# Performance work log

Hardware: AMD Instinct MI355X
Metric: run time of the kernel (lower is better)

The kernel has to match this reference:

```python
import jax, jax.numpy as jnp
import numpy as np

B, NUM_SLOTS, D, TOP_K = 2048, 128, 1024, 8
DH = D // 2  # route_mlp hidden


def setup_inputs() -> dict:
    key = jax.random.key(0)
    ks = jax.random.split(key, 16)
    s = 0.02
    return {
        "x": jax.random.normal(ks[0], (B, D), jnp.float32),
        "S": jax.random.normal(ks[1], (B, NUM_SLOTS, D), jnp.float32),
        # route_mlp: Linear(2D, D//2) -> GELU -> Linear(D//2, NUM_SLOTS)
        "w1": jax.random.normal(ks[2], (DH, 2 * D), jnp.float32) * s,
        "b1": jnp.zeros((DH,), jnp.float32),
        "w2": jax.random.normal(ks[3], (NUM_SLOTS, DH), jnp.float32) * s,
        "b2": jnp.zeros((NUM_SLOTS,), jnp.float32),
        # GRUCell(D, D): torch layout, gates ordered (r, z, n)
        "gru_wih": jax.random.normal(ks[4], (3 * D, D), jnp.float32) * s,
        "gru_whh": jax.random.normal(ks[5], (3 * D, D), jnp.float32) * s,
        "gru_bih": jnp.zeros((3 * D,), jnp.float32),
        "gru_bhh": jnp.zeros((3 * D,), jnp.float32),
        "wval": jax.random.normal(ks[6], (D, D), jnp.float32) * s,
        "bval": jnp.zeros((D,), jnp.float32),
        "wout": jax.random.normal(ks[7], (D, D), jnp.float32) * s,
        "bout": jnp.zeros((D,), jnp.float32),
        "tau": jnp.ones((1,), jnp.float32),
    }


def reference(x, S, w1, b1, w2, b2, gru_wih, gru_whh, gru_bih, gru_bhh,
              wval, bval, wout, bout, tau):
    # Routing: context = [x, mean over slots]
    slot_mean = S.mean(axis=1)                                  # [B, D]
    ctx = jnp.concatenate([x, slot_mean], axis=-1)              # [B, 2D]
    h = jax.nn.gelu(ctx @ w1.T + b1, approximate=False)         # [B, DH]
    route_logits = (h @ w2.T + b2) / (jnp.abs(tau) + 0.1)       # [B, NUM_SLOTS]

    topk_vals, topk_idx = jax.lax.top_k(route_logits, TOP_K)    # [B, K]
    topk_w = jax.nn.softmax(topk_vals, axis=-1)                 # [B, K]

    # Gather selected slot states
    slot_states = jnp.take_along_axis(S, topk_idx[:, :, None], axis=1)  # [B, K, D]

    # GRUCell (torch semantics). Input part shared across the K slots.
    gi = x @ gru_wih.T + gru_bih                                # [B, 3D]
    gh = slot_states @ gru_whh.T + gru_bhh                      # [B, K, 3D]
    gi_r, gi_z, gi_n = jnp.split(gi, 3, axis=-1)
    gh_r, gh_z, gh_n = jnp.split(gh, 3, axis=-1)
    r = jax.nn.sigmoid(gi_r[:, None, :] + gh_r)
    z = jax.nn.sigmoid(gi_z[:, None, :] + gh_z)
    n = jnp.tanh(gi_n[:, None, :] + r * gh_n)
    updated = (1.0 - z) * n + z * slot_states                   # [B, K, D]

    # Scatter updated states back into slot memory
    S_new = S.at[jnp.arange(B)[:, None], topk_idx].set(updated)

    # Weighted value readout
    values = updated @ wval.T + bval                            # [B, K, D]
    mixed = jnp.einsum('bkd,bk->bd', values, topk_w)            # [B, D]
    output = mixed @ wout.T + bout                              # [B, D]
    return output, S_new
```

## Files before the change

### kernel.cpp

```cpp
#include <hip/hip_runtime.h>
#include <math.h>
#include <stdint.h>

#define B_   2048
#define NS_  128
#define D_   1024
#define K_   8
#define DH_  512
#define G3_  3072

typedef unsigned short u16;
typedef short bf16x8 __attribute__((ext_vector_type(8)));
typedef float f32x4 __attribute__((ext_vector_type(4)));

__device__ __forceinline__ float bf2f(u16 u) {
  union { unsigned i; float f; } v; v.i = ((unsigned)u) << 16; return v.f;
}
__device__ __forceinline__ u16 f2bf(float f) {
  unsigned x = __float_as_uint(f);
  return (u16)((x + 0x7fffu + ((x >> 16) & 1u)) >> 16);
}

#define AS1C(p) ((const __attribute__((address_space(1))) void*)(uintptr_t)(p))
#define AS3(p)  ((__attribute__((address_space(3))) void*)(unsigned)(uintptr_t)(p))

template<int DO_COPY>
__global__ __launch_bounds__(256)
void sp_copyprep(const float* __restrict__ S, float* __restrict__ Snew,
                 float* __restrict__ mean,
                 const float* __restrict__ x, const float* __restrict__ wih,
                 const float* __restrict__ whh, const float* __restrict__ wout,
                 const float* __restrict__ wval, const float* __restrict__ bval,
                 const float* __restrict__ bout,
                 u16* __restrict__ xb, u16* __restrict__ wihb,
                 u16* __restrict__ whhb, u16* __restrict__ woutb,
                 u16* __restrict__ wvalT, float* __restrict__ brow) {
  __shared__ u16 tile[64][65];
  const int blk = blockIdx.x;
  const int t = threadIdx.x;
  if (blk < 2048) {
    const int b = blk;
    const int d0 = t * 4;
    const f32x4* src = (const f32x4*)(S + (size_t)b * NS_ * D_) + t;
    f32x4* dst = (f32x4*)(Snew + (size_t)b * NS_ * D_) + t;
    double a0 = 0, a1 = 0, a2 = 0, a3 = 0;
    #pragma unroll 4
    for (int s = 0; s < NS_; ++s) {
      f32x4 v = __builtin_nontemporal_load(src);
      if (DO_COPY) __builtin_nontemporal_store(v, dst);
      a0 += v[0]; a1 += v[1]; a2 += v[2]; a3 += v[3];
      src += 256; dst += 256;
    }
    float4 m;
    m.x = (float)(a0 * (1.0 / 128.0)); m.y = (float)(a1 * (1.0 / 128.0));
    m.z = (float)(a2 * (1.0 / 128.0)); m.w = (float)(a3 * (1.0 / 128.0));
    *(float4*)&mean[(size_t)b * D_ + d0] = m;
  } else if (blk < 3072) {
    const int cid = blk - 2048;
    for (int i = cid * 256 + t; i < 2359296; i += 1024 * 256) {
      const float* s; u16* d; int off;
      if (i < 524288)       { s = x;    d = xb;    off = i; }
      else if (i < 1310720) { s = wih;  d = wihb;  off = i - 524288; }
      else if (i < 2097152) { s = whh;  d = whhb;  off = i - 1310720; }
      else                  { s = wout; d = woutb; off = i - 2097152; }
      float4 v = ((const float4*)s)[off];
      ushort4 o;
      o.x = f2bf(v.x); o.y = f2bf(v.y); o.z = f2bf(v.z); o.w = f2bf(v.w);
      ((ushort4*)d)[off] = o;
    }
  } else if (blk < 3328) {
    const int tb = blk - 3072;
    const int bx = tb & 15, by = tb >> 4;
    const int r = t >> 4, c4 = (t & 15) * 4;
    #pragma unroll
    for (int p = 0; p < 4; ++p) {
      const int row = by * 64 + p * 16 + r;
      float4 v = *(const float4*)&wval[(size_t)row * D_ + bx * 64 + c4];
      tile[p * 16 + r][c4 + 0] = f2bf(v.x);
      tile[p * 16 + r][c4 + 1] = f2bf(v.y);
      tile[p * 16 + r][c4 + 2] = f2bf(v.z);
      tile[p * 16 + r][c4 + 3] = f2bf(v.w);
    }
    __syncthreads();
    #pragma unroll
    for (int p = 0; p < 4; ++p) {
      const int jr = p * 16 + r;
      ushort4 o;
      o.x = tile[c4 + 0][jr];
      o.y = tile[c4 + 1][jr];
      o.z = tile[c4 + 2][jr];
      o.w = tile[c4 + 3][jr];
      *(ushort4*)&wvalT[(size_t)(bx * 64 + jr) * D_ + by * 64 + c4] = o;
    }
  } else {
    const int w = t >> 6, l = t & 63;
    const int i = (blk - 3328) * 4 + w;
    float s = 0.f;
    const float* wr = &wout[(size_t)i * D_ + l * 16];
    const float* bv = &bval[l * 16];
    #pragma unroll
    for (int j = 0; j < 16; j += 4) {
      float4 w4 = *(const float4*)&wr[j];
      float4 b4 = *(const float4*)&bv[j];
      s += w4.x * b4.x + w4.y * b4.y + w4.z * b4.z + w4.w * b4.w;
    }
    #pragma unroll
    for (int off = 32; off > 0; off >>= 1) s += __shfl_xor(s, off);
    if (l == 0) brow[i] = s + bout[i];
  }
}

template<int EPI>
__device__ __forceinline__ void gemm_bf16_body(
    const u16* __restrict__ A, const u16* __restrict__ Bm,
    void* __restrict__ Cv, const float* __restrict__ bias,
    int M, int N, int Kd, int nbx, int wg, u16* lA, u16* lB) {
  {
    const int nwg = nbx * ((M + 127) >> 7);
    const int cpx = nwg >> 3;
    wg = (wg & 7) * cpx + (wg >> 3);
  }
  const int m0 = (wg / nbx) * 128, n0 = (wg % nbx) * 128;
  const int t = threadIdx.x;
  const int lane = t & 63;
  const int w = t >> 6;
  const int wm = w >> 1, wn = w & 1;

  f32x4 acc[4][4] = {};

  const int srow = t >> 2;
  const int scol = (t & 3) * 8;
  const u16* gA0 = A + (size_t)(m0 + srow) * Kd + scol;
  const u16* gA1 = A + (size_t)(m0 + 64 + srow) * Kd + scol;
  const u16* gB0 = Bm + (size_t)(n0 + srow) * Kd + scol;
  const u16* gB1 = Bm + (size_t)(n0 + 64 + srow) * Kd + scol;
  u16* lAw = lA + (t & 192) * 8;
  u16* lBw = lB + (t & 192) * 8;

  const int kb = (lane >> 4) * 8;
  const int rA = wm * 64 + (lane & 15);
  const int rB = wn * 64 + (lane & 15);

  for (int k0 = 0; k0 < Kd; k0 += 32) {
    __builtin_amdgcn_global_load_lds(AS1C(gA0 + k0), AS3(lAw), 16, 0, 0);
    __builtin_amdgcn_global_load_lds(AS1C(gA1 + k0), AS3(lAw + 2048), 16, 0, 0);
    __builtin_amdgcn_global_load_lds(AS1C(gB0 + k0), AS3(lBw), 16, 0, 0);
    __builtin_amdgcn_global_load_lds(AS1C(gB1 + k0), AS3(lBw + 2048), 16, 0, 0);
    __syncthreads();
    bf16x8 af[4], bfr[4];
    #pragma unroll
    for (int fm = 0; fm < 4; ++fm)
      af[fm] = *(const bf16x8*)&lA[(rA + fm * 16) * 32 + kb];
    #pragma unroll
    for (int fn = 0; fn < 4; ++fn)
      bfr[fn] = *(const bf16x8*)&lB[(rB + fn * 16) * 32 + kb];
    #pragma unroll
    for (int fm = 0; fm < 4; ++fm) {
      #pragma unroll
      for (int fn = 0; fn < 4; ++fn)
        acc[fm][fn] = __builtin_amdgcn_mfma_f32_16x16x32_bf16(af[fm], bfr[fn], acc[fm][fn], 0, 0, 0);
    }
    __syncthreads();
  }

  #pragma unroll
  for (int fm = 0; fm < 4; ++fm) {
    #pragma unroll
    for (int fn = 0; fn < 4; ++fn) {
      #pragma unroll
      for (int i = 0; i < 4; ++i) {
        const int r = m0 + wm * 64 + fm * 16 + (lane >> 4) * 4 + i;
        const int c = n0 + wn * 64 + fn * 16 + (lane & 15);
        float v = acc[fm][fn][i];
        if constexpr (EPI == 2) {
          ((float*)Cv)[(size_t)r * N + c] = v + bias[c];
        } else {
          ((u16*)Cv)[(size_t)r * N + c] = f2bf(v);
        }
      }
    }
  }
}

__global__ __launch_bounds__(256)
void sp_mid(const u16* __restrict__ xb, const u16* __restrict__ wihb,
            u16* __restrict__ gib,
            const float* __restrict__ x, const float* __restrict__ mean,
            const float* __restrict__ w1, const float* __restrict__ b1,
            float* __restrict__ h,
            const u16* __restrict__ woutb, const u16* __restrict__ wvalTb,
            u16* __restrict__ Wrob) {
  __shared__ u16 lA[128 * 32];
  __shared__ u16 lB[128 * 32];
  const int blk = blockIdx.x;
  const int t = threadIdx.x;
  if (blk < 384) {
    gemm_bf16_body<1>(xb, wihb, gib, nullptr, B_, G3_, D_, G3_ / 128, blk, lA, lB);
  } else if (blk < 640) {
    float (*As)[68] = (float(*)[68])lA;
    float (*Bs)[68] = (float(*)[68])lB;
    int wg = blk - 384;
    wg = (wg & 7) * 32 + (wg >> 3);
    const int m0 = (wg >> 3) * 64;
    const int n0 = (wg & 7) * 64;
    const int tx = t & 15, ty = t >> 4;
    float acc[4][4] = {};
    const int sr = t >> 2, sc = (t & 3) * 4;
    for (int k0 = 0; k0 < 2 * D_; k0 += 16) {
      const float* src = (k0 < D_) ? (x + k0) : (mean + (k0 - D_));
      float4 va = *(const float4*)&src[(size_t)(m0 + sr) * D_ + sc];
      As[sc + 0][sr] = va.x; As[sc + 1][sr] = va.y; As[sc + 2][sr] = va.z; As[sc + 3][sr] = va.w;
      float4 vb = *(const float4*)&w1[(size_t)(n0 + sr) * (2 * D_) + k0 + sc];
      Bs[sc + 0][sr] = vb.x; Bs[sc + 1][sr] = vb.y; Bs[sc + 2][sr] = vb.z; Bs[sc + 3][sr] = vb.w;
      __syncthreads();
      #pragma unroll
      for (int kk = 0; kk < 16; ++kk) {
        float4 a4 = *(const float4*)&As[kk][ty * 4];
        float4 b4 = *(const float4*)&Bs[kk][tx * 4];
        acc[0][0] = fmaf(a4.x, b4.x, acc[0][0]); acc[0][1] = fmaf(a4.x, b4.y, acc[0][1]);
        acc[0][2] = fmaf(a4.x, b4.z, acc[0][2]); acc[0][3] = fmaf(a4.x, b4.w, acc[0][3]);
        acc[1][0] = fmaf(a4.y, b4.x, acc[1][0]); acc[1][1] = fmaf(a4.y, b4.y, acc[1][1]);
        acc[1][2] = fmaf(a4.y, b4.z, acc[1][2]); acc[1][3] = fmaf(a4.y, b4.w, acc[1][3]);
        acc[2][0] = fmaf(a4.z, b4.x, acc[2][0]); acc[2][1] = fmaf(a4.z, b4.y, acc[2][1]);
        acc[2][2] = fmaf(a4.z, b4.z, acc[2][2]); acc[2][3] = fmaf(a4.z, b4.w, acc[2][3]);
        acc[3][0] = fmaf(a4.w, b4.x, acc[3][0]); acc[3][1] = fmaf(a4.w, b4.y, acc[3][1]);
        acc[3][2] = fmaf(a4.w, b4.z, acc[3][2]); acc[3][3] = fmaf(a4.w, b4.w, acc[3][3]);
      }
      __syncthreads();
    }
    #pragma unroll
    for (int i = 0; i < 4; ++i) {
      #pragma unroll
      for (int j = 0; j < 4; ++j) {
        const int r = m0 + ty * 4 + i, c = n0 + tx * 4 + j;
        float v = acc[i][j] + b1[c];
        v = 0.5f * v * (1.0f + erff(v * 0.70710678118654752f));
        h[(size_t)r * DH_ + c] = v;
      }
    }
  } else {
    gemm_bf16_body<1>(woutb, wvalTb, Wrob, nullptr, D_, D_, D_, 8, blk - 640, lA, lB);
  }
}

__global__ __launch_bounds__(64)
void sp_route_topk(const float* __restrict__ h, const float* __restrict__ w2,
                   const float* __restrict__ b2, const float* __restrict__ tau,
                   const float* __restrict__ S,
                   int* __restrict__ tki, float* __restrict__ tkw,
                   u16* __restrict__ slotb) {
  __shared__ float hs[DH_];
  __shared__ int sTki[K_];
  const int b = blockIdx.x, l = threadIdx.x;
  *(float4*)&hs[l * 4] = *(const float4*)&h[(size_t)b * DH_ + l * 4];
  *(float4*)&hs[256 + l * 4] = *(const float4*)&h[(size_t)b * DH_ + 256 + l * 4];
  __syncthreads();
  const double invd = 1.0 / ((double)fabsf(tau[0]) + 0.1);
  float v[2]; int id[2];
  #pragma unroll
  for (int c = 0; c < 2; ++c) {
    const int n = c * 64 + l;
    const float* wr = &w2[(size_t)n * DH_];
    double s = 0.0;
    for (int j = 0; j < DH_; j += 4) {
      float4 w4 = *(const float4*)&wr[j];
      s += (double)hs[j] * (double)w4.x;
      s += (double)hs[j + 1] * (double)w4.y;
      s += (double)hs[j + 2] * (double)w4.z;
      s += (double)hs[j + 3] * (double)w4.w;
    }
    v[c] = (float)((s + (double)b2[n]) * invd);
    id[c] = n;
  }
  float m0f = 0.f, sum = 0.f, mye = 0.f; int myi = 0;
  for (int r = 0; r < 8; ++r) {
    float mv; int mi;
    if (v[1] > v[0]) { mv = v[1]; mi = id[1]; } else { mv = v[0]; mi = id[0]; }
    #pragma unroll
    for (int off = 32; off > 0; off >>= 1) {
      float ov = __shfl_xor(mv, off);
      int oi = __shfl_xor(mi, off);
      if (ov > mv || (ov == mv && oi < mi)) { mv = ov; mi = oi; }
    }
    if (r == 0) m0f = mv;
    float er = expf(mv - m0f);
    sum += er;
    if (l == r) { mye = er; myi = mi; }
    if (mi == id[0]) v[0] = -3.0e38f;
    if (mi == id[1]) v[1] = -3.0e38f;
  }
  if (l < 8) {
    tki[b * K_ + l] = myi; tkw[b * K_ + l] = mye / sum;
    sTki[l] = myi;
  }
  __syncthreads();
  #pragma unroll
  for (int k = 0; k < K_; ++k) {
    const int s = sTki[k];
    const float4* src = (const float4*)&S[((size_t)b * NS_ + s) * D_];
    ushort4* dst = (ushort4*)&slotb[((size_t)b * K_ + k) * D_];
    #pragma unroll
    for (int c = 0; c < 4; ++c) {
      float4 vv = src[c * 64 + l];
      ushort4 o;
      o.x = f2bf(vv.x); o.y = f2bf(vv.y); o.z = f2bf(vv.z); o.w = f2bf(vv.w);
      dst[c * 64 + l] = o;
    }
  }
}

template<int EPI>
__global__ __launch_bounds__(256)
void sp_gemm_bf16(const u16* __restrict__ A, const u16* __restrict__ Bm,
                  void* __restrict__ Cv, const float* __restrict__ bias,
                  int M, int N, int Kd, int nbx) {
  __shared__ u16 lA[128 * 32];
  __shared__ u16 lB[128 * 32];
  gemm_bf16_body<EPI>(A, Bm, Cv, bias, M, N, Kd, nbx, blockIdx.x, lA, lB);
}

template<bool DIRECT>
__global__ __launch_bounds__(256, 2)
void sp_gh_gru(const u16* __restrict__ slotb, const u16* __restrict__ whhb,
               const u16* __restrict__ gib, const float* __restrict__ bih,
               const float* __restrict__ bhh, const int* __restrict__ tki,
               const float* __restrict__ tkw, float* __restrict__ dst,
               u16* __restrict__ umixb) {
  __shared__ u16 lA[128 * 32];
  __shared__ u16 lB[192 * 32];
  __shared__ int   sTki[128];
  __shared__ float sTkw[128];
  const int bidx = blockIdx.x;
  const int xcd = bidx & 7, rr = bidx >> 3;
  const int db = xcd * 2 + (rr & 1);
  const int mt = rr >> 1;
  const int m0 = mt * 128, d0 = db * 64;
  const int t = threadIdx.x;
  const int lane = t & 63, w = t >> 6;
  const int wm = w >> 1, wn = w & 1;
  const int lane15 = lane & 15, hi = lane >> 4;

  if (t < 128) { sTki[t] = tki[m0 + t]; sTkw[t] = tkw[m0 + t]; }

  f32x4 acc[4][6] = {};

  const int srow = t >> 2;
  const int scol = (t & 3) * 8;
  const u16* gA0 = slotb + (size_t)(m0 + srow) * D_ + scol;
  const u16* gA1 = slotb + (size_t)(m0 + 64 + srow) * D_ + scol;
  const u16* gB0 = whhb + (size_t)(d0 + srow) * D_ + scol;
  const u16* gB1 = whhb + (size_t)(D_ + d0 + srow) * D_ + scol;
  const u16* gB2 = whhb + (size_t)(2 * D_ + d0 + srow) * D_ + scol;
  u16* lAw = &lA[(t & 192) * 8];
  u16* lBw = &lB[(t & 192) * 8];

  const int kb = hi * 8;
  const int rA = wm * 64 + lane15;
  const int rB = wn * 32 + lane15;

  for (int k0 = 0; k0 < D_; k0 += 32) {
    __builtin_amdgcn_global_load_lds(AS1C(gA0 + k0), AS3(lAw), 16, 0, 0);
    __builtin_amdgcn_global_load_lds(AS1C(gA1 + k0), AS3(lAw + 2048), 16, 0, 0);
    __builtin_amdgcn_global_load_lds(AS1C(gB0 + k0), AS3(lBw), 16, 0, 0);
    __builtin_amdgcn_global_load_lds(AS1C(gB1 + k0), AS3(lBw + 2048), 16, 0, 0);
    __builtin_amdgcn_global_load_lds(AS1C(gB2 + k0), AS3(lBw + 4096), 16, 0, 0);
    __syncthreads();
    bf16x8 af[4], bfr[6];
    #pragma unroll
    for (int fm = 0; fm < 4; ++fm)
      af[fm] = *(const bf16x8*)&lA[(rA + fm * 16) * 32 + kb];
    #pragma unroll
    for (int g = 0; g < 3; ++g) {
      #pragma unroll
      for (int f = 0; f < 2; ++f)
        bfr[g * 2 + f] = *(const bf16x8*)&lB[(g * 64 + rB + f * 16) * 32 + kb];
    }
    #pragma unroll
    for (int fm = 0; fm < 4; ++fm) {
      #pragma unroll
      for (int fn = 0; fn < 6; ++fn)
        acc[fm][fn] = __builtin_amdgcn_mfma_f32_16x16x32_bf16(af[fm], bfr[fn], acc[fm][fn], 0, 0, 0);
    }
    __syncthreads();
  }

  #pragma unroll
  for (int fm = 0; fm < 4; ++fm) {
    const int rbase = wm * 64 + fm * 16 + hi * 4;
    const int bglob = (m0 + rbase) >> 3;
    #pragma unroll
    for (int f = 0; f < 2; ++f) {
      const int dg = d0 + wn * 32 + f * 16 + lane15;
      const float Gr = bf2f(gib[(size_t)bglob * G3_ + dg])          + bih[dg];
      const float Gz = bf2f(gib[(size_t)bglob * G3_ + D_ + dg])     + bih[D_ + dg];
      const float Gn = bf2f(gib[(size_t)bglob * G3_ + 2 * D_ + dg]) + bih[2 * D_ + dg];
      const float Br = bhh[dg], Bz = bhh[D_ + dg], Bn = bhh[2 * D_ + dg];
      float part = 0.f;
      #pragma unroll
      for (int i = 0; i < 4; ++i) {
        const int row = rbase + i;
        const int grow = m0 + row;
        const float slot = bf2f(slotb[(size_t)grow * D_ + dg]);
        const float rr2 = acc[fm][f][i] + Br;
        const float zz = acc[fm][f + 2][i] + Bz;
        const float nn = acc[fm][f + 4][i] + Bn;
        const float rg = 1.f / (1.f + expf(-(Gr + rr2)));
        const float zg = 1.f / (1.f + expf(-(Gz + zz)));
        const float ng = tanhf(Gn + rg * nn);
        const float uv = (1.f - zg) * ng + zg * slot;
        part = fmaf(sTkw[row], uv, part);
        if (DIRECT)
          __builtin_nontemporal_store(uv, &dst[((size_t)bglob * NS_ + sTki[row]) * D_ + dg]);
        else
          dst[(size_t)grow * D_ + dg] = uv;
      }
      part += __shfl_xor(part, 16);
      if ((hi & 1) == 0)
        umixb[(size_t)bglob * D_ + dg] = f2bf(part);
    }
  }
}

__global__ __launch_bounds__(256)
void sp_copy_scatter(const float* __restrict__ S, const float* __restrict__ upd,
                     const int* __restrict__ tki, float* __restrict__ Snew) {
  const int b = blockIdx.x, t = threadIdx.x;
  const int d0 = t * 4;
  int idx[K_];
  #pragma unroll
  for (int k = 0; k < K_; ++k) idx[k] = tki[b * K_ + k];
  for (int s = 0; s < NS_; ++s) {
    int sk = -1;
    #pragma unroll
    for (int k = 0; k < K_; ++k) if (idx[k] == s) sk = k;
    float4 v;
    if (sk >= 0) v = *(const float4*)&upd[((size_t)b * K_ + sk) * D_ + d0];
    else         v = *(const float4*)&S[((size_t)b * NS_ + s) * D_ + d0];
    *(float4*)&Snew[((size_t)b * NS_ + s) * D_ + d0] = v;
  }
}

extern "C" void kernel_launch(void* const* d_in, const int* in_sizes, int n_in,
                              void* d_out, int out_size, void* d_ws, size_t ws_size,
                              hipStream_t stream) {
  const float* x    = (const float*)d_in[0];
  const float* S    = (const float*)d_in[1];
  const float* w1   = (const float*)d_in[2];
  const float* b1   = (const float*)d_in[3];
  const float* w2   = (const float*)d_in[4];
  const float* b2   = (const float*)d_in[5];
  const float* wih  = (const float*)d_in[6];
  const float* whh  = (const float*)d_in[7];
  const float* bih  = (const float*)d_in[8];
  const float* bhh  = (const float*)d_in[9];
  const float* wval = (const float*)d_in[10];
  const float* bval = (const float*)d_in[11];
  const float* wout = (const float*)d_in[12];
  const float* bout = (const float*)d_in[13];
  const float* tau  = (const float*)d_in[14];

  float* out  = (float*)d_out;
  float* Snew = out + (size_t)B_ * D_;

  const bool bigws = ws_size >= (size_t)400 * 1024 * 1024;
  char* bigbase = bigws ? (char*)d_ws : (char*)Snew;
  size_t bo = 0;
  auto balloc = [&](size_t bytes) -> void* {
    void* p = bigbase + bo; bo += (bytes + 255) & ~(size_t)255; return p;
  };

  float* mean  = (float*)balloc((size_t)B_ * D_ * 4);
  float* h     = (float*)balloc((size_t)B_ * DH_ * 4);
  u16* xb      = (u16*)balloc((size_t)B_ * D_ * 2);
  u16* wihb    = (u16*)balloc((size_t)G3_ * D_ * 2);
  u16* whhb    = (u16*)balloc((size_t)G3_ * D_ * 2);
  u16* woutb   = (u16*)balloc((size_t)D_ * D_ * 2);
  u16* wvalTb  = (u16*)balloc((size_t)D_ * D_ * 2);
  u16* Wrob    = (u16*)balloc((size_t)D_ * D_ * 2);
  u16* gib     = (u16*)balloc((size_t)B_ * G3_ * 2);
  u16* slotb   = (u16*)balloc((size_t)B_ * K_ * D_ * 2);
  u16* umixb   = (u16*)balloc((size_t)B_ * D_ * 2);
  float* brow  = (float*)balloc((size_t)D_ * 4);

  char* wsb = (char*)d_ws;
  size_t so = bigws ? bo : 0;
  auto salloc = [&](size_t bytes) -> void* {
    void* p = wsb + so; so += (bytes + 255) & ~(size_t)255; return p;
  };
  int*   tki = (int*)salloc((size_t)B_ * K_ * 4);
  float* tkw = (float*)salloc((size_t)B_ * K_ * 4);
  float* upd = bigws ? nullptr : (float*)salloc((size_t)B_ * K_ * D_ * 4);

  if (bigws)
    sp_copyprep<1><<<3584, 256, 0, stream>>>(S, Snew, mean, x, wih, whh, wout,
                                             wval, bval, bout, xb, wihb, whhb,
                                             woutb, wvalTb, brow);
  else
    sp_copyprep<0><<<3584, 256, 0, stream>>>(S, Snew, mean, x, wih, whh, wout,
                                             wval, bval, bout, xb, wihb, whhb,
                                             woutb, wvalTb, brow);

  sp_mid<<<704, 256, 0, stream>>>(xb, wihb, gib, x, mean, w1, b1, h,
                                  woutb, wvalTb, Wrob);

  sp_route_topk<<<B_, 64, 0, stream>>>(h, w2, b2, tau, S, tki, tkw, slotb);

  if (bigws)
    sp_gh_gru<true><<<2048, 256, 0, stream>>>(slotb, whhb, gib, bih, bhh,
                                              tki, tkw, Snew, umixb);
  else
    sp_gh_gru<false><<<2048, 256, 0, stream>>>(slotb, whhb, gib, bih, bhh,
                                               tki, tkw, upd, umixb);

  sp_gemm_bf16<2><<<128, 256, 0, stream>>>(umixb, Wrob, out, brow, B_, D_, D_, 8);

  if (!bigws)
    sp_copy_scatter<<<B_, 256, 0, stream>>>(S, upd, tki, Snew);
}
```

Baseline: 782.4 us.

## Double-buffer LDS tiles in bf16 GEMMs and the GRU gate GEMM

Each bf16 MFMA GEMM loop (the shared GEMM body and the GRU gate GEMM) now uses two LDS buffers. It prefetches the next K-slice with global_load_lds while the current slice is being multiplied, so there is one barrier per iteration instead of two. The goal is to hide global-to-LDS latency behind MFMA work. In exchange, LDS use per block doubles, and the GRU kernel's launch-bounds occupancy hint rises from 2 to 3 blocks. That may raise register pressure, since its B fragments are now loaded per gate group inside the MFMA loop.

```diff
diff --git a/kernel.cpp b/kernel.cpp
--- a/kernel.cpp
+++ b/kernel.cpp
@@ -114,7 +114,8 @@
 __device__ __forceinline__ void gemm_bf16_body(
     const u16* __restrict__ A, const u16* __restrict__ Bm,
     void* __restrict__ Cv, const float* __restrict__ bias,
-    int M, int N, int Kd, int nbx, int wg, u16* lA, u16* lB) {
+    int M, int N, int Kd, int nbx, int wg,
+    u16* lA0, u16* lA1, u16* lB0, u16* lB1) {
   {
     const int nwg = nbx * ((M + 127) >> 7);
     const int cpx = nwg >> 3;
@@ -134,26 +135,34 @@
   const u16* gA1 = A + (size_t)(m0 + 64 + srow) * Kd + scol;
   const u16* gB0 = Bm + (size_t)(n0 + srow) * Kd + scol;
   const u16* gB1 = Bm + (size_t)(n0 + 64 + srow) * Kd + scol;
-  u16* lAw = lA + (t & 192) * 8;
-  u16* lBw = lB + (t & 192) * 8;
+  const int w16 = (t & 192) * 8;
 
   const int kb = (lane >> 4) * 8;
   const int rA = wm * 64 + (lane & 15);
   const int rB = wn * 64 + (lane & 15);
 
+  u16 *cA = lA0, *cB = lB0, *nA = lA1, *nB = lB1;
+  __builtin_amdgcn_global_load_lds(AS1C(gA0), AS3(cA + w16), 16, 0, 0);
+  __builtin_amdgcn_global_load_lds(AS1C(gA1), AS3(cA + w16 + 2048), 16, 0, 0);
+  __builtin_amdgcn_global_load_lds(AS1C(gB0), AS3(cB + w16), 16, 0, 0);
+  __builtin_amdgcn_global_load_lds(AS1C(gB1), AS3(cB + w16 + 2048), 16, 0, 0);
+  __syncthreads();
+
   for (int k0 = 0; k0 < Kd; k0 += 32) {
-    __builtin_amdgcn_global_load_lds(AS1C(gA0 + k0), AS3(lAw), 16, 0, 0);
-    __builtin_amdgcn_global_load_lds(AS1C(gA1 + k0), AS3(lAw + 2048), 16, 0, 0);
-    __builtin_amdgcn_global_load_lds(AS1C(gB0 + k0), AS3(lBw), 16, 0, 0);
-    __builtin_amdgcn_global_load_lds(AS1C(gB1 + k0), AS3(lBw + 2048), 16, 0, 0);
-    __syncthreads();
+    const int kn = k0 + 32;
+    if (kn < Kd) {
+      __builtin_amdgcn_global_load_lds(AS1C(gA0 + kn), AS3(nA + w16), 16, 0, 0);
+      __builtin_amdgcn_global_load_lds(AS1C(gA1 + kn), AS3(nA + w16 + 2048), 16, 0, 0);
+      __builtin_amdgcn_global_load_lds(AS1C(gB0 + kn), AS3(nB + w16), 16, 0, 0);
+      __builtin_amdgcn_global_load_lds(AS1C(gB1 + kn), AS3(nB + w16 + 2048), 16, 0, 0);
+    }
     bf16x8 af[4], bfr[4];
     #pragma unroll
     for (int fm = 0; fm < 4; ++fm)
-      af[fm] = *(const bf16x8*)&lA[(rA + fm * 16) * 32 + kb];
+      af[fm] = *(const bf16x8*)&cA[(rA + fm * 16) * 32 + kb];
     #pragma unroll
     for (int fn = 0; fn < 4; ++fn)
-      bfr[fn] = *(const bf16x8*)&lB[(rB + fn * 16) * 32 + kb];
+      bfr[fn] = *(const bf16x8*)&cB[(rB + fn * 16) * 32 + kb];
     #pragma unroll
     for (int fm = 0; fm < 4; ++fm) {
       #pragma unroll
@@ -161,6 +170,9 @@
         acc[fm][fn] = __builtin_amdgcn_mfma_f32_16x16x32_bf16(af[fm], bfr[fn], acc[fm][fn], 0, 0, 0);
     }
     __syncthreads();
+    u16* tp;
+    tp = cA; cA = nA; nA = tp;
+    tp = cB; cB = nB; nB = tp;
   }
 
   #pragma unroll
@@ -190,15 +202,16 @@
             float* __restrict__ h,
             const u16* __restrict__ woutb, const u16* __restrict__ wvalTb,
             u16* __restrict__ Wrob) {
-  __shared__ u16 lA[128 * 32];
-  __shared__ u16 lB[128 * 32];
+  __shared__ u16 lA[2][4096];
+  __shared__ u16 lB[2][4096];
   const int blk = blockIdx.x;
   const int t = threadIdx.x;
   if (blk < 384) {
-    gemm_bf16_body<1>(xb, wihb, gib, nullptr, B_, G3_, D_, G3_ / 128, blk, lA, lB);
+    gemm_bf16_body<1>(xb, wihb, gib, nullptr, B_, G3_, D_, G3_ / 128, blk,
+                      lA[0], lA[1], lB[0], lB[1]);
   } else if (blk < 640) {
-    float (*As)[68] = (float(*)[68])lA;
-    float (*Bs)[68] = (float(*)[68])lB;
+    float (*As)[68] = (float(*)[68])&lA[0][0];
+    float (*Bs)[68] = (float(*)[68])&lB[0][0];
     int wg = blk - 384;
     wg = (wg & 7) * 32 + (wg >> 3);
     const int m0 = (wg >> 3) * 64;
@@ -239,7 +252,8 @@
       }
     }
   } else {
-    gemm_bf16_body<1>(woutb, wvalTb, Wrob, nullptr, D_, D_, D_, 8, blk - 640, lA, lB);
+    gemm_bf16_body<1>(woutb, wvalTb, Wrob, nullptr, D_, D_, D_, 8, blk - 640,
+                      lA[0], lA[1], lB[0], lB[1]);
   }
 }
 
@@ -314,20 +328,21 @@
 void sp_gemm_bf16(const u16* __restrict__ A, const u16* __restrict__ Bm,
                   void* __restrict__ Cv, const float* __restrict__ bias,
                   int M, int N, int Kd, int nbx) {
-  __shared__ u16 lA[128 * 32];
-  __shared__ u16 lB[128 * 32];
-  gemm_bf16_body<EPI>(A, Bm, Cv, bias, M, N, Kd, nbx, blockIdx.x, lA, lB);
+  __shared__ u16 lA[2][4096];
+  __shared__ u16 lB[2][4096];
+  gemm_bf16_body<EPI>(A, Bm, Cv, bias, M, N, Kd, nbx, blockIdx.x,
+                      lA[0], lA[1], lB[0], lB[1]);
 }
 
 template<bool DIRECT>
-__global__ __launch_bounds__(256, 2)
+__global__ __launch_bounds__(256, 3)
 void sp_gh_gru(const u16* __restrict__ slotb, const u16* __restrict__ whhb,
                const u16* __restrict__ gib, const float* __restrict__ bih,
                const float* __restrict__ bhh, const int* __restrict__ tki,
                const float* __restrict__ tkw, float* __restrict__ dst,
                u16* __restrict__ umixb) {
-  __shared__ u16 lA[128 * 32];
-  __shared__ u16 lB[192 * 32];
+  __shared__ u16 lA[2][4096];
+  __shared__ u16 lB[2][6144];
   __shared__ int   sTki[128];
   __shared__ float sTkw[128];
   const int bidx = blockIdx.x;
@@ -351,37 +366,47 @@
   const u16* gB0 = whhb + (size_t)(d0 + srow) * D_ + scol;
   const u16* gB1 = whhb + (size_t)(D_ + d0 + srow) * D_ + scol;
   const u16* gB2 = whhb + (size_t)(2 * D_ + d0 + srow) * D_ + scol;
-  u16* lAw = &lA[(t & 192) * 8];
-  u16* lBw = &lB[(t & 192) * 8];
+  const int w16 = (t & 192) * 8;
 
   const int kb = hi * 8;
   const int rA = wm * 64 + lane15;
   const int rB = wn * 32 + lane15;
 
+  u16 *cA = lA[0], *cB = lB[0], *nA = lA[1], *nB = lB[1];
+  __builtin_amdgcn_global_load_lds(AS1C(gA0), AS3(cA + w16), 16, 0, 0);
+  __builtin_amdgcn_global_load_lds(AS1C(gA1), AS3(cA + w16 + 2048), 16, 0, 0);
+  __builtin_amdgcn_global_load_lds(AS1C(gB0), AS3(cB + w16), 16, 0, 0);
+  __builtin_amdgcn_global_load_lds(AS1C(gB1), AS3(cB + w16 + 2048), 16, 0, 0);
+  __builtin_amdgcn_global_load_lds(AS1C(gB2), AS3(cB + w16 + 4096), 16, 0, 0);
+  __syncthreads();
+
   for (int k0 = 0; k0 < D_; k0 += 32) {
-    __builtin_amdgcn_global_load_lds(AS1C(gA0 + k0), AS3(lAw), 16, 0, 0);
-    __builtin_amdgcn_global_load_lds(AS1C(gA1 + k0), AS3(lAw + 2048), 16, 0, 0);
-    __builtin_amdgcn_global_load_lds(AS1C(gB0 + k0), AS3(lBw), 16, 0, 0);
-    __builtin_amdgcn_global_load_lds(AS1C(gB1 + k0), AS3(lBw + 2048), 16, 0, 0);
-    __builtin_amdgcn_global_load_lds(AS1C(gB2 + k0), AS3(lBw + 4096), 16, 0, 0);
+    const int kn = k0 + 32;
+    if (kn < D_) {
+      __builtin_amdgcn_global_load_lds(AS1C(gA0 + kn), AS3(nA + w16), 16, 0, 0);
+      __builtin_amdgcn_global_load_lds(AS1C(gA1 + kn), AS3(nA + w16 + 2048), 16, 0, 0);
+      __builtin_amdgcn_global_load_lds(AS1C(gB0 + kn), AS3(nB + w16), 16, 0, 0);
+      __builtin_amdgcn_global_load_lds(AS1C(gB1 + kn), AS3(nB + w16 + 2048), 16, 0, 0);
+      __builtin_amdgcn_global_load_lds(AS1C(gB2 + kn), AS3(nB + w16 + 4096), 16, 0, 0);
+    }
+    bf16x8 af[4];
+    #pragma unroll
+    for (int fm = 0; fm < 4; ++fm)
+      af[fm] = *(const bf16x8*)&cA[(rA + fm * 16) * 32 + kb];
+    #pragma unroll
+    for (int g = 0; g < 3; ++g) {
+      bf16x8 b0 = *(const bf16x8*)&cB[(g * 64 + rB) * 32 + kb];
+      bf16x8 b1 = *(const bf16x8*)&cB[(g * 64 + rB + 16) * 32 + kb];
+      #pragma unroll
+      for (int fm = 0; fm < 4; ++fm) {
+        acc[fm][g * 2]     = __builtin_amdgcn_mfma_f32_16x16x32_bf16(af[fm], b0, acc[fm][g * 2], 0, 0, 0);
+        acc[fm][g * 2 + 1] = __builtin_amdgcn_mfma_f32_16x16x32_bf16(af[fm], b1, acc[fm][g * 2 + 1], 0, 0, 0);
+      }
+    }
     __syncthreads();
-    bf16x8 af[4], bfr[6];
-    #pragma unroll
-    for (int fm = 0; fm < 4; ++fm)
-      af[fm] = *(const bf16x8*)&lA[(rA + fm * 16) * 32 + kb];
-    #pragma unroll
-    for (int g = 0; g < 3; ++g) {
-      #pragma unroll
-      for (int f = 0; f < 2; ++f)
-        bfr[g * 2 + f] = *(const bf16x8*)&lB[(g * 64 + rB + f * 16) * 32 + kb];
-    }
-    #pragma unroll
-    for (int fm = 0; fm < 4; ++fm) {
-      #pragma unroll
-      for (int fn = 0; fn < 6; ++fn)
-        acc[fm][fn] = __builtin_amdgcn_mfma_f32_16x16x32_bf16(af[fm], bfr[fn], acc[fm][fn], 0, 0, 0);
-    }
-    __syncthreads();
+    u16* tp;
+    tp = cA; cA = nA; nA = tp;
+    tp = cB; cB = nB; nB = tp;
   }
 
   #pragma unroll
```

Result: no change. 773.5 us (-1.1%).
